# Kernel tuning notes

Measured on AMD Instinct MI355X. Metric: run time of the kernel, lower is better.

Reference implementation:

```python
import jax, jax.numpy as jnp
import numpy as np

V, H, E, L = 50257, 1024, 512, 128


def setup_inputs() -> dict:
    key = jax.random.key(0)
    ks = jax.random.split(key, 16)
    s = 0.02
    return {
        "input_tok": jax.random.randint(ks[0], (1,), 0, V),
        "h0": jax.random.normal(ks[1], (1, 1, H), jnp.float32),
        "c0": jax.random.normal(ks[2], (1, 1, H), jnp.float32),
        "enc_output": jax.random.normal(ks[3], (L, H), jnp.float32),
        "emb_table": s * jax.random.normal(ks[4], (V, E), jnp.float32),
        "attn_W": s * jax.random.normal(ks[5], (L, H + E), jnp.float32),
        "attn_b": jnp.zeros((L,), jnp.float32),
        "a2d_W": s * jax.random.normal(ks[6], (H, H + E), jnp.float32),
        "a2d_b": jnp.zeros((H,), jnp.float32),
        "W_ih": s * jax.random.normal(ks[7], (4 * H, H), jnp.float32),
        "W_hh": s * jax.random.normal(ks[8], (4 * H, H), jnp.float32),
        "b_ih": jnp.zeros((4 * H,), jnp.float32),
        "b_hh": jnp.zeros((4 * H,), jnp.float32),
        "out_W": s * jax.random.normal(ks[9], (V, H), jnp.float32),
        "out_b": jnp.zeros((V,), jnp.float32),
    }


def reference(input_tok, h0, c0, enc_output, emb_table, attn_W, attn_b,
              a2d_W, a2d_b, W_ih, W_hh, b_ih, b_hh, out_W, out_b):
    # embed: (1, E); h, c: (1, H)
    embed = emb_table[input_tok].reshape(1, E)
    h = h0.reshape(1, H)
    c = c0.reshape(1, H)
    # attention over encoder positions
    attn_in = jnp.concatenate([embed, h], axis=1)                      # (1, E+H)
    attn_weight = jax.nn.softmax(attn_in @ attn_W.T + attn_b, axis=1)  # (1, L)
    attn_out = attn_weight @ enc_output                                # (1, H)
    # combine and project to LSTM input
    dec_in = jnp.concatenate([embed, attn_out], axis=1)                # (1, E+H)
    dec_in = jax.nn.relu(dec_in @ a2d_W.T + a2d_b)                     # (1, H)
    # one LSTM cell step (torch gate order: i, f, g, o)
    gates = dec_in @ W_ih.T + b_ih + h @ W_hh.T + b_hh                 # (1, 4H)
    i_g, f_g, g_g, o_g = jnp.split(gates, 4, axis=1)
    c_new = jax.nn.sigmoid(f_g) * c + jax.nn.sigmoid(i_g) * jnp.tanh(g_g)
    h_new = jax.nn.sigmoid(o_g) * jnp.tanh(c_new)
    # output log-probs over vocab
    output = jax.nn.log_softmax(h_new @ out_W.T + out_b, axis=1)       # (1, V)
    return output, h_new.reshape(1, 1, H), c_new.reshape(1, 1, H), attn_weight
```

## Files before the change

kernel.cpp:

```cpp
#include <hip/hip_runtime.h>
#include <math.h>

#define V 50257
#define H 1024
#define E 512
#define L 128
#define HE 1536
#define NBLK5 2048

#define WS_DECRAW 0
#define WS_DECIN  1536
#define WS_HNEW   2560
#define WS_ALOGIT 3584
#define WS_PAIRS  3712

__device__ __forceinline__ float wave_reduce_sum(float v) {
    #pragma unroll
    for (int off = 32; off > 0; off >>= 1) v += __shfl_xor(v, off, 64);
    return v;
}

__global__ void k_attn_logits(const int* __restrict__ tok_p,
                              const float* __restrict__ h0,
                              const float* __restrict__ emb,
                              const float* __restrict__ attn_W,
                              const float* __restrict__ attn_b,
                              float* __restrict__ ws) {
    __shared__ __align__(16) float s_in[HE];
    const int tid = threadIdx.x;
    const int tok = tok_p[0];
    for (int k = tid; k < HE; k += 256) {
        float v = (k < E) ? emb[(size_t)tok * E + k] : h0[k - E];
        s_in[k] = v;
        if (blockIdx.x == 0 && k < E) ws[WS_DECRAW + k] = v;
    }
    __syncthreads();
    const int lane = tid & 63;
    const int gw = (blockIdx.x << 2) + (tid >> 6);
    const float4* s4 = (const float4*)s_in;
    #pragma unroll
    for (int rr = 0; rr < 2; ++rr) {
        const int r = gw * 2 + rr;
        const float4* w4 = (const float4*)(attn_W + (size_t)r * HE);
        float acc = 0.f;
        #pragma unroll
        for (int c = 0; c < 6; ++c) {
            float4 a = s4[lane + (c << 6)];
            float4 b = w4[lane + (c << 6)];
            acc = fmaf(a.x, b.x, acc); acc = fmaf(a.y, b.y, acc);
            acc = fmaf(a.z, b.z, acc); acc = fmaf(a.w, b.w, acc);
        }
        acc = wave_reduce_sum(acc);
        if (lane == 0) ws[WS_ALOGIT + r] = acc + attn_b[r];
    }
}

__global__ void k_attn_out(const float* __restrict__ enc,
                           float* __restrict__ out_attnw,
                           float* __restrict__ ws) {
    __shared__ float s_l[L];
    __shared__ float s_wn[L];
    const int tid = threadIdx.x;
    if (tid < L) s_l[tid] = ws[WS_ALOGIT + tid];
    __syncthreads();
    if (tid < L) {
        float m = -1e30f;
        for (int l = 0; l < L; ++l) m = fmaxf(m, s_l[l]);
        float s = 0.f;
        for (int l = 0; l < L; ++l) s += expf(s_l[l] - m);
        float wn = expf(s_l[tid] - m) / s;
        s_wn[tid] = wn;
        if (blockIdx.x == 0) out_attnw[tid] = wn;
    }
    __syncthreads();
    const int j = blockIdx.x * 256 + tid;
    float acc = 0.f;
    for (int l = 0; l < L; ++l) acc = fmaf(s_wn[l], enc[l * H + j], acc);
    ws[WS_DECRAW + E + j] = acc;
}

__global__ void k_a2d(const float* __restrict__ a2d_W,
                      const float* __restrict__ a2d_b,
                      float* __restrict__ ws) {
    const int lane = threadIdx.x & 63;
    const int r = (blockIdx.x << 2) + (threadIdx.x >> 6);
    const float4* x4 = (const float4*)(ws + WS_DECRAW);
    const float4* w4 = (const float4*)(a2d_W + (size_t)r * HE);
    float acc = 0.f;
    #pragma unroll
    for (int c = 0; c < 6; ++c) {
        float4 a = x4[lane + (c << 6)];
        float4 b = w4[lane + (c << 6)];
        acc = fmaf(a.x, b.x, acc); acc = fmaf(a.y, b.y, acc);
        acc = fmaf(a.z, b.z, acc); acc = fmaf(a.w, b.w, acc);
    }
    acc = wave_reduce_sum(acc);
    if (lane == 0) ws[WS_DECIN + r] = fmaxf(acc + a2d_b[r], 0.f);
}

__global__ void k_lstm(const float* __restrict__ h0,
                       const float* __restrict__ c0,
                       const float* __restrict__ W_ih,
                       const float* __restrict__ W_hh,
                       const float* __restrict__ b_ih,
                       const float* __restrict__ b_hh,
                       float* __restrict__ out_h,
                       float* __restrict__ out_c,
                       float* __restrict__ ws) {
    const int lane = threadIdx.x & 63;
    const int j = (blockIdx.x << 2) + (threadIdx.x >> 6);
    const float4* x4 = (const float4*)(ws + WS_DECIN);
    const float4* h4 = (const float4*)h0;
    float4 xr[4], hr[4];
    #pragma unroll
    for (int k = 0; k < 4; ++k) {
        xr[k] = x4[lane + (k << 6)];
        hr[k] = h4[lane + (k << 6)];
    }
    float g[4];
    #pragma unroll
    for (int gi = 0; gi < 4; ++gi) {
        const size_t r = (size_t)gi * H + j;
        const float4* wi4 = (const float4*)(W_ih + r * H);
        const float4* wh4 = (const float4*)(W_hh + r * H);
        float acc = 0.f;
        #pragma unroll
        for (int k = 0; k < 4; ++k) {
            float4 a = wi4[lane + (k << 6)];
            acc = fmaf(xr[k].x, a.x, acc); acc = fmaf(xr[k].y, a.y, acc);
            acc = fmaf(xr[k].z, a.z, acc); acc = fmaf(xr[k].w, a.w, acc);
            float4 b = wh4[lane + (k << 6)];
            acc = fmaf(hr[k].x, b.x, acc); acc = fmaf(hr[k].y, b.y, acc);
            acc = fmaf(hr[k].z, b.z, acc); acc = fmaf(hr[k].w, b.w, acc);
        }
        g[gi] = wave_reduce_sum(acc);
    }
    if (lane == 0) {
        float gi_ = g[0] + b_ih[j]         + b_hh[j];
        float gf  = g[1] + b_ih[H + j]     + b_hh[H + j];
        float gg  = g[2] + b_ih[2 * H + j] + b_hh[2 * H + j];
        float go  = g[3] + b_ih[3 * H + j] + b_hh[3 * H + j];
        float si = 1.f / (1.f + expf(-gi_));
        float sf = 1.f / (1.f + expf(-gf));
        float so = 1.f / (1.f + expf(-go));
        float cn = sf * c0[j] + si * tanhf(gg);
        float hn = so * tanhf(cn);
        out_c[j] = cn;
        out_h[j] = hn;
        ws[WS_HNEW + j] = hn;
    }
}

__global__ void k_vocab(const float* __restrict__ out_W,
                        const float* __restrict__ out_b,
                        float* __restrict__ logits,
                        float* __restrict__ ws) {
    const int lane = threadIdx.x & 63;
    const int widx = threadIdx.x >> 6;
    const int gw = (blockIdx.x << 2) + widx;
    const float4* h4 = (const float4*)(ws + WS_HNEW);
    float4 hr[4];
    #pragma unroll
    for (int k = 0; k < 4; ++k) hr[k] = h4[lane + (k << 6)];
    float m = -1e30f, s = 0.f;
    for (int v = gw; v < V; v += NBLK5 * 4) {
        const float4* w4 = (const float4*)(out_W + (size_t)v * H);
        float acc = 0.f;
        #pragma unroll
        for (int k = 0; k < 4; ++k) {
            float4 a = w4[lane + (k << 6)];
            acc = fmaf(hr[k].x, a.x, acc); acc = fmaf(hr[k].y, a.y, acc);
            acc = fmaf(hr[k].z, a.z, acc); acc = fmaf(hr[k].w, a.w, acc);
        }
        acc = wave_reduce_sum(acc);
        const float logit = acc + out_b[v];
        if (lane == 0) logits[v] = logit;
        const float mo = m;
        m = fmaxf(m, logit);
        s = s * __expf(mo - m) + __expf(logit - m);
    }
    __shared__ float sm[4], ss[4];
    if (lane == 0) { sm[widx] = m; ss[widx] = s; }
    __syncthreads();
    if (threadIdx.x == 0) {
        float M = sm[0], S = ss[0];
        #pragma unroll
        for (int i = 1; i < 4; ++i) {
            float Mn = fmaxf(M, sm[i]);
            S = S * __expf(M - Mn) + ss[i] * __expf(sm[i] - Mn);
            M = Mn;
        }
        ws[WS_PAIRS + 2 * blockIdx.x]     = M;
        ws[WS_PAIRS + 2 * blockIdx.x + 1] = S;
    }
}

__global__ void k_final(float* __restrict__ logits,
                        const float* __restrict__ ws) {
    __shared__ float sm[256], ss[256];
    const int tid = threadIdx.x;
    float M = -1e30f, S = 0.f;
    for (int i = tid; i < NBLK5; i += 256) {
        float m2 = ws[WS_PAIRS + 2 * i], s2 = ws[WS_PAIRS + 2 * i + 1];
        float Mn = fmaxf(M, m2);
        S = S * __expf(M - Mn) + s2 * __expf(m2 - Mn);
        M = Mn;
    }
    sm[tid] = M; ss[tid] = S;
    __syncthreads();
    for (int off = 128; off > 0; off >>= 1) {
        if (tid < off) {
            float m2 = sm[tid + off], s2 = ss[tid + off];
            float Mn = fmaxf(sm[tid], m2);
            ss[tid] = ss[tid] * __expf(sm[tid] - Mn) + s2 * __expf(m2 - Mn);
            sm[tid] = Mn;
        }
        __syncthreads();
    }
    const float C = sm[0] + logf(ss[0]);
    for (int v = blockIdx.x * 256 + tid; v < V; v += gridDim.x * 256)
        logits[v] -= C;
}

extern "C" void kernel_launch(void* const* d_in, const int* in_sizes, int n_in,
                              void* d_out, int out_size, void* d_ws, size_t ws_size,
                              hipStream_t stream) {
    const int*   tok    = (const int*)d_in[0];
    const float* h0     = (const float*)d_in[1];
    const float* c0     = (const float*)d_in[2];
    const float* enc    = (const float*)d_in[3];
    const float* emb    = (const float*)d_in[4];
    const float* attn_W = (const float*)d_in[5];
    const float* attn_b = (const float*)d_in[6];
    const float* a2d_W  = (const float*)d_in[7];
    const float* a2d_b  = (const float*)d_in[8];
    const float* W_ih   = (const float*)d_in[9];
    const float* W_hh   = (const float*)d_in[10];
    const float* b_ih   = (const float*)d_in[11];
    const float* b_hh   = (const float*)d_in[12];
    const float* out_W  = (const float*)d_in[13];
    const float* out_b  = (const float*)d_in[14];

    float* out        = (float*)d_out;
    float* ws         = (float*)d_ws;
    float* out_logits = out;
    float* out_h      = out + V;
    float* out_c      = out + V + H;
    float* out_attnw  = out + V + 2 * H;

    k_attn_logits<<<16, 256, 0, stream>>>(tok, h0, emb, attn_W, attn_b, ws);
    k_attn_out<<<4, 256, 0, stream>>>(enc, out_attnw, ws);
    k_a2d<<<256, 256, 0, stream>>>(a2d_W, a2d_b, ws);
    k_lstm<<<256, 256, 0, stream>>>(h0, c0, W_ih, W_hh, b_ih, b_hh, out_h, out_c, ws);
    k_vocab<<<NBLK5, 256, 0, stream>>>(out_W, out_b, out_logits, ws);
    k_final<<<256, 256, 0, stream>>>(out_logits, ws);
}
```

Before: 71.61 us.

## Spread small GEMV stages across more blocks and stream weights with nontemporal loads

The attention-logit, a2d and LSTM kernels now give each output row its own block, with waves splitting the dot product and reducing through shared memory. This raises parallelism in these latency-bound stages. The attention-output kernel splits the L reduction across four waves and uses 16 blocks. The vocab and LSTM kernels load weights with nontemporal hints, and the vocab loop handles two rows per iteration to keep more loads in flight. The cost is extra block-level syncs and more launched blocks, and the softmax now uses the fast __expf.

```diff
diff --git a/kernel.cpp b/kernel.cpp
--- a/kernel.cpp
+++ b/kernel.cpp
@@ -7,6 +7,7 @@
 #define L 128
 #define HE 1536
 #define NBLK5 2048
+#define VSTRIDE (NBLK5 * 4)
 
 #define WS_DECRAW 0
 #define WS_DECIN  1536
@@ -14,10 +15,17 @@
 #define WS_ALOGIT 3584
 #define WS_PAIRS  3712
 
+typedef float f32x4 __attribute__((ext_vector_type(4)));
+
 __device__ __forceinline__ float wave_reduce_sum(float v) {
     #pragma unroll
     for (int off = 32; off > 0; off >>= 1) v += __shfl_xor(v, off, 64);
     return v;
+}
+
+__device__ __forceinline__ float4 ntload(const float4* p) {
+    f32x4 r = __builtin_nontemporal_load((const f32x4*)p);
+    return make_float4(r.x, r.y, r.z, r.w);
 }
 
 __global__ void k_attn_logits(const int* __restrict__ tok_p,
@@ -27,75 +35,86 @@
                               const float* __restrict__ attn_b,
                               float* __restrict__ ws) {
     __shared__ __align__(16) float s_in[HE];
+    __shared__ float s_part[6];
     const int tid = threadIdx.x;
     const int tok = tok_p[0];
-    for (int k = tid; k < HE; k += 256) {
+    for (int k = tid; k < HE; k += 384) {
         float v = (k < E) ? emb[(size_t)tok * E + k] : h0[k - E];
         s_in[k] = v;
         if (blockIdx.x == 0 && k < E) ws[WS_DECRAW + k] = v;
     }
     __syncthreads();
-    const int lane = tid & 63;
-    const int gw = (blockIdx.x << 2) + (tid >> 6);
+    const int lane = tid & 63, w = tid >> 6;
+    const int r = blockIdx.x;
     const float4* s4 = (const float4*)s_in;
-    #pragma unroll
-    for (int rr = 0; rr < 2; ++rr) {
-        const int r = gw * 2 + rr;
-        const float4* w4 = (const float4*)(attn_W + (size_t)r * HE);
-        float acc = 0.f;
-        #pragma unroll
-        for (int c = 0; c < 6; ++c) {
-            float4 a = s4[lane + (c << 6)];
-            float4 b = w4[lane + (c << 6)];
-            acc = fmaf(a.x, b.x, acc); acc = fmaf(a.y, b.y, acc);
-            acc = fmaf(a.z, b.z, acc); acc = fmaf(a.w, b.w, acc);
-        }
-        acc = wave_reduce_sum(acc);
-        if (lane == 0) ws[WS_ALOGIT + r] = acc + attn_b[r];
+    const float4* w4 = (const float4*)(attn_W + (size_t)r * HE);
+    float4 a = s4[lane + (w << 6)];
+    float4 b = w4[lane + (w << 6)];
+    float acc = a.x * b.x + a.y * b.y + a.z * b.z + a.w * b.w;
+    acc = wave_reduce_sum(acc);
+    if (lane == 0) s_part[w] = acc;
+    __syncthreads();
+    if (tid == 0) {
+        float t = s_part[0] + s_part[1] + s_part[2] + s_part[3] + s_part[4] + s_part[5];
+        ws[WS_ALOGIT + r] = t + attn_b[r];
     }
 }
 
 __global__ void k_attn_out(const float* __restrict__ enc,
                            float* __restrict__ out_attnw,
                            float* __restrict__ ws) {
-    __shared__ float s_l[L];
     __shared__ float s_wn[L];
+    __shared__ float s_acc[4][64];
     const int tid = threadIdx.x;
-    if (tid < L) s_l[tid] = ws[WS_ALOGIT + tid];
+    if (tid < L) s_wn[tid] = ws[WS_ALOGIT + tid];
+    __syncthreads();
+    float m = -1e30f;
+    #pragma unroll
+    for (int l = 0; l < L; ++l) m = fmaxf(m, s_wn[l]);
+    float s = 0.f;
+    #pragma unroll
+    for (int l = 0; l < L; ++l) s += __expf(s_wn[l] - m);
     __syncthreads();
     if (tid < L) {
-        float m = -1e30f;
-        for (int l = 0; l < L; ++l) m = fmaxf(m, s_l[l]);
-        float s = 0.f;
-        for (int l = 0; l < L; ++l) s += expf(s_l[l] - m);
-        float wn = expf(s_l[tid] - m) / s;
+        float wn = __expf(s_wn[tid] - m) / s;
         s_wn[tid] = wn;
         if (blockIdx.x == 0) out_attnw[tid] = wn;
     }
     __syncthreads();
-    const int j = blockIdx.x * 256 + tid;
+    const int j = blockIdx.x * 64 + (tid & 63);
+    const int lg = tid >> 6;
     float acc = 0.f;
-    for (int l = 0; l < L; ++l) acc = fmaf(s_wn[l], enc[l * H + j], acc);
-    ws[WS_DECRAW + E + j] = acc;
+    #pragma unroll
+    for (int li = 0; li < 32; ++li) {
+        const int l = (lg << 5) + li;
+        acc = fmaf(s_wn[l], enc[l * H + j], acc);
+    }
+    s_acc[lg][tid & 63] = acc;
+    __syncthreads();
+    if (tid < 64) {
+        float r = s_acc[0][tid] + s_acc[1][tid] + s_acc[2][tid] + s_acc[3][tid];
+        ws[WS_DECRAW + E + blockIdx.x * 64 + tid] = r;
+    }
 }
 
 __global__ void k_a2d(const float* __restrict__ a2d_W,
                       const float* __restrict__ a2d_b,
                       float* __restrict__ ws) {
-    const int lane = threadIdx.x & 63;
-    const int r = (blockIdx.x << 2) + (threadIdx.x >> 6);
+    __shared__ float s_part[6];
+    const int tid = threadIdx.x, lane = tid & 63, w = tid >> 6;
+    const int r = blockIdx.x;
     const float4* x4 = (const float4*)(ws + WS_DECRAW);
     const float4* w4 = (const float4*)(a2d_W + (size_t)r * HE);
-    float acc = 0.f;
-    #pragma unroll
-    for (int c = 0; c < 6; ++c) {
-        float4 a = x4[lane + (c << 6)];
-        float4 b = w4[lane + (c << 6)];
-        acc = fmaf(a.x, b.x, acc); acc = fmaf(a.y, b.y, acc);
-        acc = fmaf(a.z, b.z, acc); acc = fmaf(a.w, b.w, acc);
-    }
+    float4 a = x4[lane + (w << 6)];
+    float4 b = w4[lane + (w << 6)];
+    float acc = a.x * b.x + a.y * b.y + a.z * b.z + a.w * b.w;
     acc = wave_reduce_sum(acc);
-    if (lane == 0) ws[WS_DECIN + r] = fmaxf(acc + a2d_b[r], 0.f);
+    if (lane == 0) s_part[w] = acc;
+    __syncthreads();
+    if (tid == 0) {
+        float t = s_part[0] + s_part[1] + s_part[2] + s_part[3] + s_part[4] + s_part[5];
+        ws[WS_DECIN + r] = fmaxf(t + a2d_b[r], 0.f);
+    }
 }
 
 __global__ void k_lstm(const float* __restrict__ h0,
@@ -107,39 +126,34 @@
                        float* __restrict__ out_h,
                        float* __restrict__ out_c,
                        float* __restrict__ ws) {
-    const int lane = threadIdx.x & 63;
-    const int j = (blockIdx.x << 2) + (threadIdx.x >> 6);
+    __shared__ float s_g[4];
+    const int tid = threadIdx.x, lane = tid & 63, w = tid >> 6;
+    const int j = blockIdx.x;
     const float4* x4 = (const float4*)(ws + WS_DECIN);
     const float4* h4 = (const float4*)h0;
-    float4 xr[4], hr[4];
+    const size_t r = (size_t)w * H + j;
+    const float4* wi4 = (const float4*)(W_ih + r * H);
+    const float4* wh4 = (const float4*)(W_hh + r * H);
+    float acc = 0.f;
     #pragma unroll
     for (int k = 0; k < 4; ++k) {
-        xr[k] = x4[lane + (k << 6)];
-        hr[k] = h4[lane + (k << 6)];
-    }
-    float g[4];
-    #pragma unroll
-    for (int gi = 0; gi < 4; ++gi) {
-        const size_t r = (size_t)gi * H + j;
-        const float4* wi4 = (const float4*)(W_ih + r * H);
-        const float4* wh4 = (const float4*)(W_hh + r * H);
-        float acc = 0.f;
-        #pragma unroll
-        for (int k = 0; k < 4; ++k) {
-            float4 a = wi4[lane + (k << 6)];
-            acc = fmaf(xr[k].x, a.x, acc); acc = fmaf(xr[k].y, a.y, acc);
-            acc = fmaf(xr[k].z, a.z, acc); acc = fmaf(xr[k].w, a.w, acc);
-            float4 b = wh4[lane + (k << 6)];
-            acc = fmaf(hr[k].x, b.x, acc); acc = fmaf(hr[k].y, b.y, acc);
-            acc = fmaf(hr[k].z, b.z, acc); acc = fmaf(hr[k].w, b.w, acc);
-        }
-        g[gi] = wave_reduce_sum(acc);
-    }
-    if (lane == 0) {
-        float gi_ = g[0] + b_ih[j]         + b_hh[j];
-        float gf  = g[1] + b_ih[H + j]     + b_hh[H + j];
-        float gg  = g[2] + b_ih[2 * H + j] + b_hh[2 * H + j];
-        float go  = g[3] + b_ih[3 * H + j] + b_hh[3 * H + j];
+        float4 a = ntload(wi4 + lane + (k << 6));
+        float4 x = x4[lane + (k << 6)];
+        acc = fmaf(a.x, x.x, acc); acc = fmaf(a.y, x.y, acc);
+        acc = fmaf(a.z, x.z, acc); acc = fmaf(a.w, x.w, acc);
+        float4 b = ntload(wh4 + lane + (k << 6));
+        float4 h = h4[lane + (k << 6)];
+        acc = fmaf(b.x, h.x, acc); acc = fmaf(b.y, h.y, acc);
+        acc = fmaf(b.z, h.z, acc); acc = fmaf(b.w, h.w, acc);
+    }
+    acc = wave_reduce_sum(acc);
+    if (lane == 0) s_g[w] = acc;
+    __syncthreads();
+    if (tid == 0) {
+        float gi_ = s_g[0] + b_ih[j]         + b_hh[j];
+        float gf  = s_g[1] + b_ih[H + j]     + b_hh[H + j];
+        float gg  = s_g[2] + b_ih[2 * H + j] + b_hh[2 * H + j];
+        float go  = s_g[3] + b_ih[3 * H + j] + b_hh[3 * H + j];
         float si = 1.f / (1.f + expf(-gi_));
         float sf = 1.f / (1.f + expf(-gf));
         float so = 1.f / (1.f + expf(-go));
@@ -163,21 +177,39 @@
     #pragma unroll
     for (int k = 0; k < 4; ++k) hr[k] = h4[lane + (k << 6)];
     float m = -1e30f, s = 0.f;
-    for (int v = gw; v < V; v += NBLK5 * 4) {
-        const float4* w4 = (const float4*)(out_W + (size_t)v * H);
-        float acc = 0.f;
+    for (int v = gw; v < V; v += 2 * VSTRIDE) {
+        const int v2 = v + VSTRIDE;
+        const float4* w0 = (const float4*)(out_W + (size_t)v * H);
+        float acc0 = 0.f, acc1 = 0.f;
         #pragma unroll
         for (int k = 0; k < 4; ++k) {
-            float4 a = w4[lane + (k << 6)];
-            acc = fmaf(hr[k].x, a.x, acc); acc = fmaf(hr[k].y, a.y, acc);
-            acc = fmaf(hr[k].z, a.z, acc); acc = fmaf(hr[k].w, a.w, acc);
-        }
-        acc = wave_reduce_sum(acc);
-        const float logit = acc + out_b[v];
-        if (lane == 0) logits[v] = logit;
-        const float mo = m;
-        m = fmaxf(m, logit);
-        s = s * __expf(mo - m) + __expf(logit - m);
+            float4 a = ntload(w0 + lane + (k << 6));
+            acc0 = fmaf(hr[k].x, a.x, acc0); acc0 = fmaf(hr[k].y, a.y, acc0);
+            acc0 = fmaf(hr[k].z, a.z, acc0); acc0 = fmaf(hr[k].w, a.w, acc0);
+        }
+        if (v2 < V) {
+            const float4* w1 = (const float4*)(out_W + (size_t)v2 * H);
+            #pragma unroll
+            for (int k = 0; k < 4; ++k) {
+                float4 a = ntload(w1 + lane + (k << 6));
+                acc1 = fmaf(hr[k].x, a.x, acc1); acc1 = fmaf(hr[k].y, a.y, acc1);
+                acc1 = fmaf(hr[k].z, a.z, acc1); acc1 = fmaf(hr[k].w, a.w, acc1);
+            }
+        }
+        acc0 = wave_reduce_sum(acc0);
+        float l0 = acc0 + out_b[v];
+        if (lane == 0) logits[v] = l0;
+        float mo = m;
+        m = fmaxf(m, l0);
+        s = s * __expf(mo - m) + __expf(l0 - m);
+        if (v2 < V) {
+            acc1 = wave_reduce_sum(acc1);
+            float l1 = acc1 + out_b[v2];
+            if (lane == 0) logits[v2] = l1;
+            mo = m;
+            m = fmaxf(m, l1);
+            s = s * __expf(mo - m) + __expf(l1 - m);
+        }
     }
     __shared__ float sm[4], ss[4];
     if (lane == 0) { sm[widx] = m; ss[widx] = s; }
@@ -248,10 +280,10 @@
     float* out_c      = out + V + H;
     float* out_attnw  = out + V + 2 * H;
 
-    k_attn_logits<<<16, 256, 0, stream>>>(tok, h0, emb, attn_W, attn_b, ws);
-    k_attn_out<<<4, 256, 0, stream>>>(enc, out_attnw, ws);
-    k_a2d<<<256, 256, 0, stream>>>(a2d_W, a2d_b, ws);
-    k_lstm<<<256, 256, 0, stream>>>(h0, c0, W_ih, W_hh, b_ih, b_hh, out_h, out_c, ws);
+    k_attn_logits<<<128, 384, 0, stream>>>(tok, h0, emb, attn_W, attn_b, ws);
+    k_attn_out<<<16, 256, 0, stream>>>(enc, out_attnw, ws);
+    k_a2d<<<1024, 384, 0, stream>>>(a2d_W, a2d_b, ws);
+    k_lstm<<<1024, 256, 0, stream>>>(h0, c0, W_ih, W_hh, b_ih, b_hh, out_h, out_c, ws);
     k_vocab<<<NBLK5, 256, 0, stream>>>(out_W, out_b, out_logits, ws);
     k_final<<<256, 256, 0, stream>>>(out_logits, ws);
 }
```

Measured after the change: 65.36 us. -8.7%, faster.
